# Optimization experiments

Measured on AMD Instinct MI355X. Metric: run time of the kernel, lower is better.

## Reference

```python
import jax, jax.numpy as jnp
import numpy as np
import math

E = 1024   # embed_dim
H = 16     # num_heads
LAT = 1024 # latent_dim
P = LAT // 16  # projectionMatrice output dim (per-head width)
B = 2
S = 2048


def setup_inputs() -> dict:
    key = jax.random.key(0)
    ks = jax.random.split(key, 11)
    sc = 0.02  # small init scale so exp(dot(q_vec, k_vec)) stays finite
    return {
        "x": jax.random.normal(ks[0], (B, S, E), jnp.float32),
        "WQ": jax.random.normal(ks[1], (E, E), jnp.float32) * sc,
        "WK": jax.random.normal(ks[2], (E, E), jnp.float32) * sc,
        "WV": jax.random.normal(ks[3], (E, E), jnp.float32) * sc,
        "result_weight": jax.random.normal(ks[4], (E, E), jnp.float32) * sc,
        "proj_w": jax.random.normal(ks[5], (E, P), jnp.float32) * sc,
        "proj_b": jax.random.normal(ks[6], (P,), jnp.float32) * sc,
        "q1_vector": jax.random.normal(ks[7], (E,), jnp.float32) * sc,
        "k1_vector": jax.random.normal(ks[8], (E,), jnp.float32) * sc,
        "q2_vector": jax.random.normal(ks[9], (E,), jnp.float32) * sc,
        "k2_vector": jax.random.normal(ks[10], (E,), jnp.float32) * sc,
        "lambda_init": jnp.zeros((1,), jnp.float32),
    }


def reference(x, WQ, WK, WV, result_weight, proj_w, proj_b,
              q1_vector, k1_vector, q2_vector, k2_vector, lambda_init):
    head_dim = E // H
    scale = 1.0 / math.sqrt(head_dim)
    # projectionMatrice(x @ W): torch Linear -> x @ proj_w + proj_b with proj_w [E, P]
    q = (x @ WQ) @ proj_w + proj_b   # [B, S, P]
    k = (x @ WK) @ proj_w + proj_b   # [B, S, P]
    v = (x @ WV) @ proj_w + proj_b   # [B, S, P]
    q1, q2 = jnp.split(q, 2, axis=-1)  # [B, S, P/2] each
    k1, k2 = jnp.split(k, 2, axis=-1)
    lam = (jnp.exp(jnp.dot(q1_vector, k1_vector))
           - jnp.exp(jnp.dot(q2_vector, k2_vector)) + lambda_init[0])
    attn1 = jnp.einsum('bsp,btp->bst', q1, k1) * scale  # [B, S, S]
    attn2 = jnp.einsum('bsp,btp->bst', q2, k2) * scale
    base = jnp.einsum('bst,btp->bsp', attn1 - lam * attn2, v)  # [B, S, P]
    # Stateful KV-cache grows by one identical (key, value) copy per head call;
    # head i's tiled-cache output equals (i+1) * base (exact reassociation).
    mult = jnp.arange(1, H + 1, dtype=x.dtype)  # [H]
    heads = (base[:, :, None, :] * mult[None, None, :, None]).reshape(B, S, H * P)  # [B, S, E]
    return heads @ result_weight
```

## Files before the change

kernel.cpp:

```cpp
#include <hip/hip_runtime.h>
#include <hip/hip_bf16.h>


typedef __attribute__((ext_vector_type(8))) short short8;
typedef __attribute__((ext_vector_type(4))) float f32x4;
typedef unsigned short ushort_t;
typedef unsigned int uint_t;

__device__ inline ushort_t f2bf(float v) {
    uint_t u = __float_as_uint(v);
    return (ushort_t)((u + 0x7FFF + ((u >> 16) & 1)) >> 16);
}
__device__ inline float bf2f(ushort_t h) { return __uint_as_float(((uint_t)h) << 16); }
__device__ inline void split2(float v, ushort_t& hi, ushort_t& lo) {
    hi = f2bf(v);
    lo = f2bf(v - bf2f(hi));
}
__device__ inline int swzA(int row, int k) { return (row * 64 + k) ^ ((row & 7) << 3); }

#define WS_PTRS(ws) \
    float* wppartT = (ws); \
    float* qpart   = (ws) + 1572864; \
    float* Mpart   = (ws) + 7864320; \
    float* Weff    = (ws) + 8388608; \
    float* lamp    = (ws) + 8454144; \
    ushort_t* ub   = (ushort_t*)((ws) + 8454160); \
    ushort_t* WpThi = ub; \
    ushort_t* WpTlo = ub + 196608; \
    ushort_t* Qhi   = ub + 393216; \
    ushort_t* Qlo   = ub + 655360; \
    ushort_t* GThi  = ub + 917504; \
    ushort_t* GTlo  = ub + 1048576;

__global__ __launch_bounds__(256) void mla_p1(
    const float* __restrict__ WQ, const float* __restrict__ WK, const float* __restrict__ WV,
    const float* __restrict__ proj_w, const float* __restrict__ RW,
    const float* __restrict__ q1v, const float* __restrict__ k1v,
    const float* __restrict__ q2v, const float* __restrict__ k2v,
    const float* __restrict__ lam0, float* __restrict__ ws)
{
    __shared__ __align__(16) char smem[32768];
    WS_PTRS(ws)
    (void)qpart; (void)Mpart; (void)WpThi; (void)WpTlo; (void)Qhi; (void)Qlo; (void)GThi; (void)GTlo;
    int t = blockIdx.x, tid = threadIdx.x;
    int wave = tid >> 6, lane = tid & 63, rl = lane & 15, kg = lane >> 4;

    if (t < 384) {
        ushort_t* Ah = (ushort_t*)smem;
        ushort_t* Al = (ushort_t*)(smem + 8192);
        ushort_t* Bh = (ushort_t*)(smem + 16384);
        ushort_t* Bl = (ushort_t*)(smem + 24576);
        int slice = t / 48, tt = t % 48, z = tt / 16, rowblk = tt % 16;
        const float* A = ((z == 0) ? WQ : (z == 1) ? WK : WV) + (long long)rowblk * 64 * 1024;
        f32x4 acc[4] = {};
        int k0 = slice * 128;
        for (int ch = 0; ch < 2; ++ch, k0 += 64) {
            #pragma unroll
            for (int i = 0; i < 4; ++i) {
                int pos = tid + 256 * i;
                int r = pos >> 4, k4 = (pos & 15) * 4;
                float4 v = *(const float4*)&A[(long long)r * 1024 + k0 + k4];
                ushort4 h, l;
                split2(v.x, h.x, l.x); split2(v.y, h.y, l.y);
                split2(v.z, h.z, l.z); split2(v.w, h.w, l.w);
                int idx = swzA(r, k4);
                *(ushort4*)&Ah[idx] = h;
                *(ushort4*)&Al[idx] = l;
            }
            #pragma unroll
            for (int i = 0; i < 4; ++i) {
                int pos = tid + 256 * i;
                int kk = pos >> 4, n4 = (pos & 15) * 4;
                float4 v = *(const float4*)&proj_w[(long long)(k0 + kk) * 64 + n4];
                float vv[4] = {v.x, v.y, v.z, v.w};
                #pragma unroll
                for (int j = 0; j < 4; ++j) {
                    ushort_t h, l; split2(vv[j], h, l);
                    int idx = swzA(n4 + j, kk);
                    Bh[idx] = h; Bl[idx] = l;
                }
            }
            __syncthreads();
            int ar = wave * 16 + rl;
            #pragma unroll
            for (int ks = 0; ks < 2; ++ks) {
                int kb = ks * 32 + kg * 8;
                short8 ah = *(const short8*)&Ah[swzA(ar, kb)];
                short8 al = *(const short8*)&Al[swzA(ar, kb)];
                #pragma unroll
                for (int n = 0; n < 4; ++n) {
                    int bi = swzA(n * 16 + rl, kb);
                    short8 bh = *(const short8*)&Bh[bi];
                    short8 bl = *(const short8*)&Bl[bi];
                    acc[n] = __builtin_amdgcn_mfma_f32_16x16x32_bf16(ah, bh, acc[n], 0, 0, 0);
                    acc[n] = __builtin_amdgcn_mfma_f32_16x16x32_bf16(ah, bl, acc[n], 0, 0, 0);
                    acc[n] = __builtin_amdgcn_mfma_f32_16x16x32_bf16(al, bh, acc[n], 0, 0, 0);
                }
            }
            __syncthreads();
        }
        #pragma unroll
        for (int n = 0; n < 4; ++n) {
            int col = n * 16 + rl;
            float4 o = {acc[n][0], acc[n][1], acc[n][2], acc[n][3]};
            long long idx = (long long)slice * 196608 + (long long)(z * 64 + col) * 1024
                          + rowblk * 64 + wave * 16 + kg * 4;
            *(float4*)&wppartT[idx] = o;
        }
    } else if (t < 448) {
        int f4i = (t - 384) * 256 + tid;
        int p = f4i >> 8, e4 = (f4i & 255) * 4;
        float4 s = {0.f, 0.f, 0.f, 0.f};
        #pragma unroll
        for (int h = 0; h < 16; ++h) {
            float4 r = *(const float4*)&RW[(long long)(h * 64 + p) * 1024 + e4];
            float m = (float)(h + 1);
            s.x += m * r.x; s.y += m * r.y; s.z += m * r.z; s.w += m * r.w;
        }
        *(float4*)&Weff[(long long)p * 1024 + e4] = s;
    } else {
        float* red = (float*)smem;
        float d1 = 0.f, d2 = 0.f;
        for (int i = tid; i < 1024; i += 256) {
            d1 += q1v[i] * k1v[i];
            d2 += q2v[i] * k2v[i];
        }
        #pragma unroll
        for (int off = 32; off > 0; off >>= 1) {
            d1 += __shfl_down(d1, off);
            d2 += __shfl_down(d2, off);
        }
        if ((tid & 63) == 0) { red[tid >> 6] = d1; red[4 + (tid >> 6)] = d2; }
        __syncthreads();
        if (tid == 0) {
            float s1 = red[0] + red[1] + red[2] + red[3];
            float s2 = red[4] + red[5] + red[6] + red[7];
            lamp[0] = expf(s1) - expf(s2) + lam0[0];
        }
    }
}

__global__ __launch_bounds__(256) void mla_p2(float* __restrict__ ws)
{
    WS_PTRS(ws)
    (void)qpart; (void)Mpart; (void)Weff; (void)lamp; (void)Qhi; (void)Qlo; (void)GThi; (void)GTlo;
    int idx = blockIdx.x * 256 + threadIdx.x;
    long long off = (long long)idx * 4;
    float4 s = {0.f, 0.f, 0.f, 0.f};
    #pragma unroll
    for (int sl = 0; sl < 8; ++sl) {
        float4 m = *(const float4*)&wppartT[(long long)sl * 196608 + off];
        s.x += m.x; s.y += m.y; s.z += m.z; s.w += m.w;
    }
    ushort4 h, l;
    split2(s.x, h.x, l.x); split2(s.y, h.y, l.y);
    split2(s.z, h.z, l.z); split2(s.w, h.w, l.w);
    *(ushort4*)&WpThi[off] = h;
    *(ushort4*)&WpTlo[off] = l;
}

__global__ __launch_bounds__(256) void mla_p3(const float* __restrict__ x, float* __restrict__ ws)
{
    __shared__ __align__(16) char smem[65536];
    WS_PTRS(ws)
    (void)wppartT; (void)Mpart; (void)Weff; (void)lamp; (void)Qhi; (void)Qlo; (void)GThi; (void)GTlo;
    ushort_t* Ah = (ushort_t*)smem;
    ushort_t* Al = (ushort_t*)(smem + 8192);
    ushort_t (*Bh)[4096] = (ushort_t(*)[4096])(smem + 16384);
    ushort_t (*Bl)[4096] = (ushort_t(*)[4096])(smem + 40960);
    int t = blockIdx.x, tid = threadIdx.x;
    int wave = tid >> 6, lane = tid & 63, rl = lane & 15, kg = lane >> 4;
    int rowblk = t & 63, slice = t >> 6;
    long long row0 = (long long)rowblk * 64;
    f32x4 acc[3][4] = {};
    int k0 = slice * 128;
    for (int ch = 0; ch < 2; ++ch, k0 += 64) {
        #pragma unroll
        for (int i = 0; i < 4; ++i) {
            int pos = tid + 256 * i;
            int r = pos >> 4, k4 = (pos & 15) * 4;
            float4 v = *(const float4*)&x[(row0 + r) * 1024 + k0 + k4];
            ushort4 h, l;
            split2(v.x, h.x, l.x); split2(v.y, h.y, l.y);
            split2(v.z, h.z, l.z); split2(v.w, h.w, l.w);
            int idx = swzA(r, k4);
            *(ushort4*)&Ah[idx] = h;
            *(ushort4*)&Al[idx] = l;
        }
        #pragma unroll
        for (int z = 0; z < 3; ++z) {
            #pragma unroll
            for (int i = 0; i < 2; ++i) {
                int pos = tid + 256 * i;
                int n = pos >> 3, k8 = (pos & 7) * 8;
                int idx = swzA(n, k8);
                long long src = (long long)(z * 64 + n) * 1024 + k0 + k8;
                *(short8*)&Bh[z][idx] = *(const short8*)&WpThi[src];
                *(short8*)&Bl[z][idx] = *(const short8*)&WpTlo[src];
            }
        }
        __syncthreads();
        int ar = wave * 16 + rl;
        #pragma unroll
        for (int ks = 0; ks < 2; ++ks) {
            int kb = ks * 32 + kg * 8;
            short8 ah = *(const short8*)&Ah[swzA(ar, kb)];
            short8 al = *(const short8*)&Al[swzA(ar, kb)];
            #pragma unroll
            for (int z = 0; z < 3; ++z) {
                #pragma unroll
                for (int n = 0; n < 4; ++n) {
                    int bi = swzA(n * 16 + rl, kb);
                    short8 bh = *(const short8*)&Bh[z][bi];
                    short8 bl = *(const short8*)&Bl[z][bi];
                    acc[z][n] = __builtin_amdgcn_mfma_f32_16x16x32_bf16(ah, bh, acc[z][n], 0, 0, 0);
                    acc[z][n] = __builtin_amdgcn_mfma_f32_16x16x32_bf16(ah, bl, acc[z][n], 0, 0, 0);
                    acc[z][n] = __builtin_amdgcn_mfma_f32_16x16x32_bf16(al, bh, acc[z][n], 0, 0, 0);
                }
            }
        }
        __syncthreads();
    }
    #pragma unroll
    for (int z = 0; z < 3; ++z) {
        float* C = qpart + (long long)(slice * 3 + z) * 262144;
        #pragma unroll
        for (int n = 0; n < 4; ++n) {
            int col = n * 16 + rl;
            #pragma unroll
            for (int j = 0; j < 4; ++j) {
                long long row = row0 + wave * 16 + kg * 4 + j;
                C[row * 64 + col] = acc[z][n][j];
            }
        }
    }
}

__global__ __launch_bounds__(256) void mla_p4(const float* __restrict__ proj_b, float* __restrict__ ws)
{
    __shared__ __align__(16) char smem[17408];
    WS_PTRS(ws)
    (void)wppartT; (void)Weff; (void)lamp; (void)WpThi; (void)WpTlo; (void)GThi; (void)GTlo;
    int t = blockIdx.x, tid = threadIdx.x;
    if (t < 128) {
        float (*ksh)[68] = (float(*)[68])smem;
        float (*vsh)[68] = (float(*)[68])(smem + 8704);
        int sc = t & 63, b = t >> 6;
        long long row0 = (long long)b * 2048 + sc * 32;
        #pragma unroll
        for (int i = 0; i < 4; ++i) {
            int pos = tid + 256 * i;
            int arr = pos >> 9, rem = pos & 511;
            int r = rem >> 4, c4 = (rem & 15) * 4;
            float4 s = *(const float4*)&proj_b[c4];
            long long off = (row0 + r) * 64 + c4;
            #pragma unroll
            for (int sl = 0; sl < 8; ++sl) {
                float4 m = *(const float4*)&qpart[(long long)(sl * 3 + 1 + arr) * 262144 + off];
                s.x += m.x; s.y += m.y; s.z += m.z; s.w += m.w;
            }
            if (arr == 0) *(float4*)&ksh[r][c4] = s;
            else          *(float4*)&vsh[r][c4] = s;
        }
        __syncthreads();
        int p = tid & 63, cgi = tid >> 6;
        float macc[16] = {};
        for (int s = 0; s < 32; ++s) {
            float vv = vsh[s][p];
            float4 k0 = *(const float4*)&ksh[s][cgi * 16];
            float4 k1 = *(const float4*)&ksh[s][cgi * 16 + 4];
            float4 k2 = *(const float4*)&ksh[s][cgi * 16 + 8];
            float4 k3 = *(const float4*)&ksh[s][cgi * 16 + 12];
            macc[0] += k0.x * vv;  macc[1] += k0.y * vv;  macc[2] += k0.z * vv;  macc[3] += k0.w * vv;
            macc[4] += k1.x * vv;  macc[5] += k1.y * vv;  macc[6] += k1.z * vv;  macc[7] += k1.w * vv;
            macc[8] += k2.x * vv;  macc[9] += k2.y * vv;  macc[10] += k2.z * vv; macc[11] += k2.w * vv;
            macc[12] += k3.x * vv; macc[13] += k3.y * vv; macc[14] += k3.z * vv; macc[15] += k3.w * vv;
        }
        float* o = Mpart + ((long long)b * 64 + sc) * 4096;
        #pragma unroll
        for (int ci = 0; ci < 16; ++ci)
            o[(cgi * 16 + ci) * 64 + p] = macc[ci];
    } else {
        int qb = t - 128;
        long long row0 = (long long)qb * 128;
        #pragma unroll
        for (int i = 0; i < 8; ++i) {
            int pos = tid + 256 * i;
            int r = pos >> 4, c4 = (pos & 15) * 4;
            float4 s = *(const float4*)&proj_b[c4];
            long long off = (row0 + r) * 64 + c4;
            #pragma unroll
            for (int sl = 0; sl < 8; ++sl) {
                float4 m = *(const float4*)&qpart[(long long)(sl * 3) * 262144 + off];
                s.x += m.x; s.y += m.y; s.z += m.z; s.w += m.w;
            }
            ushort4 h, l;
            split2(s.x, h.x, l.x); split2(s.y, h.y, l.y);
            split2(s.z, h.z, l.z); split2(s.w, h.w, l.w);
            *(ushort4*)&Qhi[off] = h;
            *(ushort4*)&Qlo[off] = l;
        }
    }
}

__global__ __launch_bounds__(256) void mla_p5(float* __restrict__ ws)
{
    __shared__ __align__(16) char smem[34816];
    WS_PTRS(ws)
    (void)wppartT; (void)qpart; (void)WpThi; (void)WpTlo; (void)Qhi; (void)Qlo;
    float (*As)[68] = (float(*)[68])smem;
    float (*Bs)[68] = (float(*)[68])(smem + 17408);
    int t = blockIdx.x, tid = threadIdx.x;
    int colblk = t & 15, b = t >> 4;
    float lam = lamp[0];
    #pragma unroll
    for (int i = 0; i < 4; ++i) {
        int pos = tid + 256 * i;
        int c = pos >> 4, p4 = (pos & 15) * 4;
        float4 s = {0.f, 0.f, 0.f, 0.f};
        #pragma unroll 8
        for (int sc = 0; sc < 64; ++sc) {
            float4 m = *(const float4*)&Mpart[((long long)b * 64 + sc) * 4096 + c * 64 + p4];
            s.x += m.x; s.y += m.y; s.z += m.z; s.w += m.w;
        }
        float coef = 0.125f * (c < 32 ? 1.0f : -lam);
        s.x *= coef; s.y *= coef; s.z *= coef; s.w *= coef;
        *(float4*)&As[c][p4] = s;
    }
    #pragma unroll
    for (int i = 0; i < 4; ++i) {
        int pos = tid + 256 * i;
        int p = pos >> 4, e4 = (pos & 15) * 4;
        *(float4*)&Bs[p][e4] = *(const float4*)&Weff[(long long)p * 1024 + colblk * 64 + e4];
    }
    __syncthreads();
    int tx = tid & 15, ty = tid >> 4;
    float acc[4][4] = {};
    #pragma unroll 4
    for (int kk4 = 0; kk4 < 64; kk4 += 4) {
        float4 a4[4], b4[4];
        #pragma unroll
        for (int i = 0; i < 4; ++i) a4[i] = *(const float4*)&As[ty * 4 + i][kk4];
        #pragma unroll
        for (int r = 0; r < 4; ++r) b4[r] = *(const float4*)&Bs[kk4 + r][tx * 4];
        #pragma unroll
        for (int i = 0; i < 4; ++i) {
            acc[i][0] += a4[i].x * b4[0].x + a4[i].y * b4[1].x + a4[i].z * b4[2].x + a4[i].w * b4[3].x;
            acc[i][1] += a4[i].x * b4[0].y + a4[i].y * b4[1].y + a4[i].z * b4[2].y + a4[i].w * b4[3].y;
            acc[i][2] += a4[i].x * b4[0].z + a4[i].y * b4[1].z + a4[i].z * b4[2].z + a4[i].w * b4[3].z;
            acc[i][3] += a4[i].x * b4[0].w + a4[i].y * b4[1].w + a4[i].z * b4[2].w + a4[i].w * b4[3].w;
        }
    }
    #pragma unroll
    for (int i = 0; i < 4; ++i)
        #pragma unroll
        for (int j = 0; j < 4; ++j) {
            ushort_t h, l; split2(acc[i][j], h, l);
            long long idx = (long long)b * 65536 + (long long)(colblk * 64 + tx * 4 + j) * 64 + ty * 4 + i;
            GThi[idx] = h; GTlo[idx] = l;
        }
}

__global__ __launch_bounds__(256) void mla_p6(float* __restrict__ ws, float* __restrict__ out)
{
    __shared__ __align__(16) char smem[32768];
    WS_PTRS(ws)
    (void)wppartT; (void)qpart; (void)Mpart; (void)Weff; (void)lamp; (void)WpThi; (void)WpTlo;
    ushort_t* Ah = (ushort_t*)smem;
    ushort_t* Al = (ushort_t*)(smem + 8192);
    ushort_t* Bh = (ushort_t*)(smem + 16384);
    ushort_t* Bl = (ushort_t*)(smem + 24576);
    int t = blockIdx.x, tid = threadIdx.x;
    int wave = tid >> 6, lane = tid & 63, rl = lane & 15, kg = lane >> 4;
    int rowblk = t & 31, colblk = (t >> 5) & 15, b = t >> 9;
    long long row0 = (long long)b * 2048 + rowblk * 64;
    #pragma unroll
    for (int i = 0; i < 2; ++i) {
        int pos = tid + 256 * i;
        int n = pos >> 3, k8 = (pos & 7) * 8;
        int idx = swzA(n, k8);
        long long qsrc = (row0 + n) * 64 + k8;
        long long gsrc = (long long)b * 65536 + (long long)(colblk * 64 + n) * 64 + k8;
        *(short8*)&Ah[idx] = *(const short8*)&Qhi[qsrc];
        *(short8*)&Al[idx] = *(const short8*)&Qlo[qsrc];
        *(short8*)&Bh[idx] = *(const short8*)&GThi[gsrc];
        *(short8*)&Bl[idx] = *(const short8*)&GTlo[gsrc];
    }
    __syncthreads();
    f32x4 acc[4] = {};
    int ar = wave * 16 + rl;
    #pragma unroll
    for (int ks = 0; ks < 2; ++ks) {
        int kb = ks * 32 + kg * 8;
        short8 ah = *(const short8*)&Ah[swzA(ar, kb)];
        short8 al = *(const short8*)&Al[swzA(ar, kb)];
        #pragma unroll
        for (int n = 0; n < 4; ++n) {
            int bi = swzA(n * 16 + rl, kb);
            short8 bh = *(const short8*)&Bh[bi];
            short8 bl = *(const short8*)&Bl[bi];
            acc[n] = __builtin_amdgcn_mfma_f32_16x16x32_bf16(ah, bh, acc[n], 0, 0, 0);
            acc[n] = __builtin_amdgcn_mfma_f32_16x16x32_bf16(ah, bl, acc[n], 0, 0, 0);
            acc[n] = __builtin_amdgcn_mfma_f32_16x16x32_bf16(al, bh, acc[n], 0, 0, 0);
        }
    }
    #pragma unroll
    for (int n = 0; n < 4; ++n) {
        int col = colblk * 64 + n * 16 + rl;
        #pragma unroll
        for (int j = 0; j < 4; ++j) {
            int row = rowblk * 64 + wave * 16 + kg * 4 + j;
            out[(long long)b * 2097152 + (long long)row * 1024 + col] = acc[n][j];
        }
    }
}

extern "C" void kernel_launch(void* const* d_in, const int* in_sizes, int n_in,
                              void* d_out, int out_size, void* d_ws, size_t ws_size,
                              hipStream_t stream)
{
    const float* x      = (const float*)d_in[0];
    const float* WQ     = (const float*)d_in[1];
    const float* WK     = (const float*)d_in[2];
    const float* WV     = (const float*)d_in[3];
    const float* RW     = (const float*)d_in[4];
    const float* proj_w = (const float*)d_in[5];
    const float* proj_b = (const float*)d_in[6];
    const float* q1v    = (const float*)d_in[7];
    const float* k1v    = (const float*)d_in[8];
    const float* q2v    = (const float*)d_in[9];
    const float* k2v    = (const float*)d_in[10];
    const float* lam0   = (const float*)d_in[11];
    float* ws  = (float*)d_ws;
    float* out = (float*)d_out;

    dim3 blk(256);
    mla_p1<<<dim3(449), blk, 0, stream>>>(WQ, WK, WV, proj_w, RW,
                                          q1v, k1v, q2v, k2v, lam0, ws);
    mla_p2<<<dim3(192), blk, 0, stream>>>(ws);
    mla_p3<<<dim3(512), blk, 0, stream>>>(x, ws);
    mla_p4<<<dim3(160), blk, 0, stream>>>(proj_b, ws);
    mla_p5<<<dim3(32), blk, 0, stream>>>(ws);
    mla_p6<<<dim3(1024), blk, 0, stream>>>(ws, out);
}
```

Before: 67.62 us.

## Rebalance kernel split, prefetch QKV projection tiles into registers, halve split-K slices

The Wp^T reduction moves into the same launch as the Weff and lambda work, and the first kernel keeps only the WQ/WK/WV×proj_w split-K GEMM. The x·Wp GEMM now uses 4 K-slices of 256 instead of 8 of 128, and it prefetches the next x and Wp tiles into registers while MFMAs run on the current tile. The M-partial kernel now covers 64 rows per block, which halves the number of partials that the G kernel reduces. Fewer, larger blocks cut partial-sum traffic and expose load latency less often, but they reduce parallelism across CUs and add register pressure.

```diff
diff --git a/kernel.cpp b/kernel.cpp
--- a/kernel.cpp
+++ b/kernel.cpp
@@ -21,10 +21,10 @@
 #define WS_PTRS(ws) \
     float* wppartT = (ws); \
     float* qpart   = (ws) + 1572864; \
-    float* Mpart   = (ws) + 7864320; \
-    float* Weff    = (ws) + 8388608; \
-    float* lamp    = (ws) + 8454144; \
-    ushort_t* ub   = (ushort_t*)((ws) + 8454160); \
+    float* Mpart   = (ws) + 4718592; \
+    float* Weff    = (ws) + 4980736; \
+    float* lamp    = (ws) + 5046272; \
+    ushort_t* ub   = (ushort_t*)((ws) + 5046288); \
     ushort_t* WpThi = ub; \
     ushort_t* WpTlo = ub + 196608; \
     ushort_t* Qhi   = ub + 393216; \
@@ -32,154 +32,30 @@
     ushort_t* GThi  = ub + 917504; \
     ushort_t* GTlo  = ub + 1048576;
 
-__global__ __launch_bounds__(256) void mla_p1(
+__global__ __launch_bounds__(256) void prep_sk(
     const float* __restrict__ WQ, const float* __restrict__ WK, const float* __restrict__ WV,
-    const float* __restrict__ proj_w, const float* __restrict__ RW,
-    const float* __restrict__ q1v, const float* __restrict__ k1v,
-    const float* __restrict__ q2v, const float* __restrict__ k2v,
-    const float* __restrict__ lam0, float* __restrict__ ws)
-{
-    __shared__ __align__(16) char smem[32768];
-    WS_PTRS(ws)
-    (void)qpart; (void)Mpart; (void)WpThi; (void)WpTlo; (void)Qhi; (void)Qlo; (void)GThi; (void)GTlo;
-    int t = blockIdx.x, tid = threadIdx.x;
-    int wave = tid >> 6, lane = tid & 63, rl = lane & 15, kg = lane >> 4;
-
-    if (t < 384) {
-        ushort_t* Ah = (ushort_t*)smem;
-        ushort_t* Al = (ushort_t*)(smem + 8192);
-        ushort_t* Bh = (ushort_t*)(smem + 16384);
-        ushort_t* Bl = (ushort_t*)(smem + 24576);
-        int slice = t / 48, tt = t % 48, z = tt / 16, rowblk = tt % 16;
-        const float* A = ((z == 0) ? WQ : (z == 1) ? WK : WV) + (long long)rowblk * 64 * 1024;
-        f32x4 acc[4] = {};
-        int k0 = slice * 128;
-        for (int ch = 0; ch < 2; ++ch, k0 += 64) {
-            #pragma unroll
-            for (int i = 0; i < 4; ++i) {
-                int pos = tid + 256 * i;
-                int r = pos >> 4, k4 = (pos & 15) * 4;
-                float4 v = *(const float4*)&A[(long long)r * 1024 + k0 + k4];
-                ushort4 h, l;
-                split2(v.x, h.x, l.x); split2(v.y, h.y, l.y);
-                split2(v.z, h.z, l.z); split2(v.w, h.w, l.w);
-                int idx = swzA(r, k4);
-                *(ushort4*)&Ah[idx] = h;
-                *(ushort4*)&Al[idx] = l;
-            }
-            #pragma unroll
-            for (int i = 0; i < 4; ++i) {
-                int pos = tid + 256 * i;
-                int kk = pos >> 4, n4 = (pos & 15) * 4;
-                float4 v = *(const float4*)&proj_w[(long long)(k0 + kk) * 64 + n4];
-                float vv[4] = {v.x, v.y, v.z, v.w};
-                #pragma unroll
-                for (int j = 0; j < 4; ++j) {
-                    ushort_t h, l; split2(vv[j], h, l);
-                    int idx = swzA(n4 + j, kk);
-                    Bh[idx] = h; Bl[idx] = l;
-                }
-            }
-            __syncthreads();
-            int ar = wave * 16 + rl;
-            #pragma unroll
-            for (int ks = 0; ks < 2; ++ks) {
-                int kb = ks * 32 + kg * 8;
-                short8 ah = *(const short8*)&Ah[swzA(ar, kb)];
-                short8 al = *(const short8*)&Al[swzA(ar, kb)];
-                #pragma unroll
-                for (int n = 0; n < 4; ++n) {
-                    int bi = swzA(n * 16 + rl, kb);
-                    short8 bh = *(const short8*)&Bh[bi];
-                    short8 bl = *(const short8*)&Bl[bi];
-                    acc[n] = __builtin_amdgcn_mfma_f32_16x16x32_bf16(ah, bh, acc[n], 0, 0, 0);
-                    acc[n] = __builtin_amdgcn_mfma_f32_16x16x32_bf16(ah, bl, acc[n], 0, 0, 0);
-                    acc[n] = __builtin_amdgcn_mfma_f32_16x16x32_bf16(al, bh, acc[n], 0, 0, 0);
-                }
-            }
-            __syncthreads();
-        }
-        #pragma unroll
-        for (int n = 0; n < 4; ++n) {
-            int col = n * 16 + rl;
-            float4 o = {acc[n][0], acc[n][1], acc[n][2], acc[n][3]};
-            long long idx = (long long)slice * 196608 + (long long)(z * 64 + col) * 1024
-                          + rowblk * 64 + wave * 16 + kg * 4;
-            *(float4*)&wppartT[idx] = o;
-        }
-    } else if (t < 448) {
-        int f4i = (t - 384) * 256 + tid;
-        int p = f4i >> 8, e4 = (f4i & 255) * 4;
-        float4 s = {0.f, 0.f, 0.f, 0.f};
-        #pragma unroll
-        for (int h = 0; h < 16; ++h) {
-            float4 r = *(const float4*)&RW[(long long)(h * 64 + p) * 1024 + e4];
-            float m = (float)(h + 1);
-            s.x += m * r.x; s.y += m * r.y; s.z += m * r.z; s.w += m * r.w;
-        }
-        *(float4*)&Weff[(long long)p * 1024 + e4] = s;
-    } else {
-        float* red = (float*)smem;
-        float d1 = 0.f, d2 = 0.f;
-        for (int i = tid; i < 1024; i += 256) {
-            d1 += q1v[i] * k1v[i];
-            d2 += q2v[i] * k2v[i];
-        }
-        #pragma unroll
-        for (int off = 32; off > 0; off >>= 1) {
-            d1 += __shfl_down(d1, off);
-            d2 += __shfl_down(d2, off);
-        }
-        if ((tid & 63) == 0) { red[tid >> 6] = d1; red[4 + (tid >> 6)] = d2; }
-        __syncthreads();
-        if (tid == 0) {
-            float s1 = red[0] + red[1] + red[2] + red[3];
-            float s2 = red[4] + red[5] + red[6] + red[7];
-            lamp[0] = expf(s1) - expf(s2) + lam0[0];
-        }
-    }
-}
-
-__global__ __launch_bounds__(256) void mla_p2(float* __restrict__ ws)
-{
-    WS_PTRS(ws)
-    (void)qpart; (void)Mpart; (void)Weff; (void)lamp; (void)Qhi; (void)Qlo; (void)GThi; (void)GTlo;
-    int idx = blockIdx.x * 256 + threadIdx.x;
-    long long off = (long long)idx * 4;
-    float4 s = {0.f, 0.f, 0.f, 0.f};
-    #pragma unroll
-    for (int sl = 0; sl < 8; ++sl) {
-        float4 m = *(const float4*)&wppartT[(long long)sl * 196608 + off];
-        s.x += m.x; s.y += m.y; s.z += m.z; s.w += m.w;
-    }
-    ushort4 h, l;
-    split2(s.x, h.x, l.x); split2(s.y, h.y, l.y);
-    split2(s.z, h.z, l.z); split2(s.w, h.w, l.w);
-    *(ushort4*)&WpThi[off] = h;
-    *(ushort4*)&WpTlo[off] = l;
-}
-
-__global__ __launch_bounds__(256) void mla_p3(const float* __restrict__ x, float* __restrict__ ws)
-{
-    __shared__ __align__(16) char smem[65536];
-    WS_PTRS(ws)
-    (void)wppartT; (void)Mpart; (void)Weff; (void)lamp; (void)Qhi; (void)Qlo; (void)GThi; (void)GTlo;
-    ushort_t* Ah = (ushort_t*)smem;
-    ushort_t* Al = (ushort_t*)(smem + 8192);
-    ushort_t (*Bh)[4096] = (ushort_t(*)[4096])(smem + 16384);
-    ushort_t (*Bl)[4096] = (ushort_t(*)[4096])(smem + 40960);
-    int t = blockIdx.x, tid = threadIdx.x;
-    int wave = tid >> 6, lane = tid & 63, rl = lane & 15, kg = lane >> 4;
-    int rowblk = t & 63, slice = t >> 6;
-    long long row0 = (long long)rowblk * 64;
-    f32x4 acc[3][4] = {};
+    const float* __restrict__ proj_w, float* __restrict__ ws)
+{
+    __shared__ __align__(16) ushort_t Ah[4096], Al[4096], Bh[4096], Bl[4096];
+    WS_PTRS(ws)
+    (void)qpart; (void)Mpart; (void)Weff; (void)lamp;
+    (void)WpThi; (void)WpTlo; (void)Qhi; (void)Qlo; (void)GThi; (void)GTlo;
+    int bid = blockIdx.x;
+    int slice = bid / 48, t = bid % 48, z = t / 16, rowblk = t % 16;
+    const float* A = ((z == 0) ? WQ : (z == 1) ? WK : WV) + (long long)rowblk * 64 * 1024;
+
+    int tid = threadIdx.x;
+    int wave = tid >> 6, lane = tid & 63;
+    int rl = lane & 15, kg = lane >> 4;
+    f32x4 acc[4] = {};
+
     int k0 = slice * 128;
     for (int ch = 0; ch < 2; ++ch, k0 += 64) {
         #pragma unroll
         for (int i = 0; i < 4; ++i) {
             int pos = tid + 256 * i;
             int r = pos >> 4, k4 = (pos & 15) * 4;
-            float4 v = *(const float4*)&x[(row0 + r) * 1024 + k0 + k4];
+            float4 v = *(const float4*)&A[(long long)r * 1024 + k0 + k4];
             ushort4 h, l;
             split2(v.x, h.x, l.x); split2(v.y, h.y, l.y);
             split2(v.z, h.z, l.z); split2(v.w, h.w, l.w);
@@ -188,18 +64,181 @@
             *(ushort4*)&Al[idx] = l;
         }
         #pragma unroll
-        for (int z = 0; z < 3; ++z) {
+        for (int i = 0; i < 4; ++i) {
+            int pos = tid + 256 * i;
+            int kk = pos >> 4, n4 = (pos & 15) * 4;
+            float4 v = *(const float4*)&proj_w[(long long)(k0 + kk) * 64 + n4];
+            float vv[4] = {v.x, v.y, v.z, v.w};
+            #pragma unroll
+            for (int j = 0; j < 4; ++j) {
+                ushort_t h, l; split2(vv[j], h, l);
+                int idx = swzA(n4 + j, kk);
+                Bh[idx] = h; Bl[idx] = l;
+            }
+        }
+        __syncthreads();
+        int ar = wave * 16 + rl;
+        #pragma unroll
+        for (int ks = 0; ks < 2; ++ks) {
+            int kb = ks * 32 + kg * 8;
+            short8 ah = *(const short8*)&Ah[swzA(ar, kb)];
+            short8 al = *(const short8*)&Al[swzA(ar, kb)];
+            #pragma unroll
+            for (int n = 0; n < 4; ++n) {
+                int bi = swzA(n * 16 + rl, kb);
+                short8 bh = *(const short8*)&Bh[bi];
+                short8 bl = *(const short8*)&Bl[bi];
+                acc[n] = __builtin_amdgcn_mfma_f32_16x16x32_bf16(ah, bh, acc[n], 0, 0, 0);
+                acc[n] = __builtin_amdgcn_mfma_f32_16x16x32_bf16(ah, bl, acc[n], 0, 0, 0);
+                acc[n] = __builtin_amdgcn_mfma_f32_16x16x32_bf16(al, bh, acc[n], 0, 0, 0);
+            }
+        }
+        __syncthreads();
+    }
+    #pragma unroll
+    for (int n = 0; n < 4; ++n) {
+        int col = n * 16 + rl;
+        float4 o = {acc[n][0], acc[n][1], acc[n][2], acc[n][3]};
+        long long idx = (long long)slice * 196608 + (long long)(z * 64 + col) * 1024
+                      + rowblk * 64 + wave * 16 + kg * 4;
+        *(float4*)&wppartT[idx] = o;
+    }
+}
+
+__global__ __launch_bounds__(256) void wpfix2x(
+    const float* __restrict__ RW,
+    const float* __restrict__ q1v, const float* __restrict__ k1v,
+    const float* __restrict__ q2v, const float* __restrict__ k2v,
+    const float* __restrict__ lam0, float* __restrict__ ws)
+{
+    __shared__ float red[2][4];
+    WS_PTRS(ws)
+    (void)qpart; (void)Mpart; (void)Qhi; (void)Qlo; (void)GThi; (void)GTlo;
+    int t = blockIdx.x, tid = threadIdx.x;
+    if (t < 192) {
+        int idx = t * 256 + tid;
+        long long off = (long long)idx * 4;
+        float4 s = {0.f, 0.f, 0.f, 0.f};
+        #pragma unroll
+        for (int sl = 0; sl < 8; ++sl) {
+            float4 m = *(const float4*)&wppartT[(long long)sl * 196608 + off];
+            s.x += m.x; s.y += m.y; s.z += m.z; s.w += m.w;
+        }
+        ushort4 h, l;
+        split2(s.x, h.x, l.x); split2(s.y, h.y, l.y);
+        split2(s.z, h.z, l.z); split2(s.w, h.w, l.w);
+        *(ushort4*)&WpThi[off] = h;
+        *(ushort4*)&WpTlo[off] = l;
+    } else if (t < 256) {
+        int f4i = (t - 192) * 256 + tid;
+        int p = f4i >> 8, e4 = (f4i & 255) * 4;
+        float4 s = {0.f, 0.f, 0.f, 0.f};
+        #pragma unroll
+        for (int h = 0; h < 16; ++h) {
+            float4 r = *(const float4*)&RW[(long long)(h * 64 + p) * 1024 + e4];
+            float m = (float)(h + 1);
+            s.x += m * r.x; s.y += m * r.y; s.z += m * r.z; s.w += m * r.w;
+        }
+        *(float4*)&Weff[(long long)p * 1024 + e4] = s;
+    } else {
+        float d1 = 0.f, d2 = 0.f;
+        for (int i = tid; i < 1024; i += 256) {
+            d1 += q1v[i] * k1v[i];
+            d2 += q2v[i] * k2v[i];
+        }
+        #pragma unroll
+        for (int off = 32; off > 0; off >>= 1) {
+            d1 += __shfl_down(d1, off);
+            d2 += __shfl_down(d2, off);
+        }
+        if ((tid & 63) == 0) { red[0][tid >> 6] = d1; red[1][tid >> 6] = d2; }
+        __syncthreads();
+        if (tid == 0) {
+            float s1 = red[0][0] + red[0][1] + red[0][2] + red[0][3];
+            float s2 = red[1][0] + red[1][1] + red[1][2] + red[1][3];
+            lamp[0] = expf(s1) - expf(s2) + lam0[0];
+        }
+    }
+}
+
+__global__ __launch_bounds__(256) void qkv_f(
+    const float* __restrict__ x, float* __restrict__ ws)
+{
+    __shared__ __align__(16) char smem[65536];
+    WS_PTRS(ws)
+    (void)wppartT; (void)Mpart; (void)Weff; (void)lamp; (void)Qhi; (void)Qlo; (void)GThi; (void)GTlo;
+    ushort_t* Ah = (ushort_t*)smem;
+    ushort_t* Al = (ushort_t*)(smem + 8192);
+    ushort_t (*Bh)[4096] = (ushort_t(*)[4096])(smem + 16384);
+    ushort_t (*Bl)[4096] = (ushort_t(*)[4096])(smem + 40960);
+    int bid = blockIdx.x, tid = threadIdx.x;
+    int wave = tid >> 6, lane = tid & 63, rl = lane & 15, kg = lane >> 4;
+    int rowblk = bid & 63, slice = bid >> 6;
+    long long row0 = (long long)rowblk * 64;
+    f32x4 acc[3][4] = {};
+
+    float4 av[4];
+    short8 pbh[3][2], pbl[3][2];
+    int k0 = slice * 256;
+    #pragma unroll
+    for (int i = 0; i < 4; ++i) {
+        int pos = tid + 256 * i;
+        int r = pos >> 4, k4 = (pos & 15) * 4;
+        av[i] = *(const float4*)&x[(row0 + r) * 1024 + k0 + k4];
+    }
+    #pragma unroll
+    for (int z = 0; z < 3; ++z)
+        #pragma unroll
+        for (int i = 0; i < 2; ++i) {
+            int pos = tid + 256 * i;
+            int n = pos >> 3, k8 = (pos & 7) * 8;
+            long long src = (long long)(z * 64 + n) * 1024 + k0 + k8;
+            pbh[z][i] = *(const short8*)&WpThi[src];
+            pbl[z][i] = *(const short8*)&WpTlo[src];
+        }
+
+    for (int ch = 0; ch < 4; ++ch) {
+        #pragma unroll
+        for (int i = 0; i < 4; ++i) {
+            int pos = tid + 256 * i;
+            int r = pos >> 4, k4 = (pos & 15) * 4;
+            ushort4 h, l;
+            split2(av[i].x, h.x, l.x); split2(av[i].y, h.y, l.y);
+            split2(av[i].z, h.z, l.z); split2(av[i].w, h.w, l.w);
+            int idx = swzA(r, k4);
+            *(ushort4*)&Ah[idx] = h;
+            *(ushort4*)&Al[idx] = l;
+        }
+        #pragma unroll
+        for (int z = 0; z < 3; ++z)
             #pragma unroll
             for (int i = 0; i < 2; ++i) {
                 int pos = tid + 256 * i;
                 int n = pos >> 3, k8 = (pos & 7) * 8;
                 int idx = swzA(n, k8);
-                long long src = (long long)(z * 64 + n) * 1024 + k0 + k8;
-                *(short8*)&Bh[z][idx] = *(const short8*)&WpThi[src];
-                *(short8*)&Bl[z][idx] = *(const short8*)&WpTlo[src];
-            }
-        }
+                *(short8*)&Bh[z][idx] = pbh[z][i];
+                *(short8*)&Bl[z][idx] = pbl[z][i];
+            }
         __syncthreads();
+        if (ch < 3) {
+            int kn = k0 + (ch + 1) * 64;
+            #pragma unroll
+            for (int i = 0; i < 4; ++i) {
+                int pos = tid + 256 * i;
+                int r = pos >> 4, k4 = (pos & 15) * 4;
+                av[i] = *(const float4*)&x[(row0 + r) * 1024 + kn + k4];
+            }
+            #pragma unroll
+            for (int z = 0; z < 3; ++z)
+                #pragma unroll
+                for (int i = 0; i < 2; ++i) {
+                    int pos = tid + 256 * i;
+                    int n = pos >> 3, k8 = (pos & 7) * 8;
+                    long long src = (long long)(z * 64 + n) * 1024 + kn + k8;
+                    pbh[z][i] = *(const short8*)&WpThi[src];
+                    pbl[z][i] = *(const short8*)&WpTlo[src];
+                }
+        }
         int ar = wave * 16 + rl;
         #pragma unroll
         for (int ks = 0; ks < 2; ++ks) {
@@ -219,7 +258,7 @@
                 }
             }
         }
-        __syncthreads();
+        __builtin_amdgcn_s_barrier();
     }
     #pragma unroll
     for (int z = 0; z < 3; ++z) {
@@ -236,26 +275,27 @@
     }
 }
 
-__global__ __launch_bounds__(256) void mla_p4(const float* __restrict__ proj_b, float* __restrict__ ws)
-{
-    __shared__ __align__(16) char smem[17408];
+__global__ __launch_bounds__(256) void mpartq(
+    const float* __restrict__ proj_b, float* __restrict__ ws)
+{
+    __shared__ __align__(16) char smem[34816];
     WS_PTRS(ws)
     (void)wppartT; (void)Weff; (void)lamp; (void)WpThi; (void)WpTlo; (void)GThi; (void)GTlo;
     int t = blockIdx.x, tid = threadIdx.x;
-    if (t < 128) {
+    if (t < 64) {
         float (*ksh)[68] = (float(*)[68])smem;
-        float (*vsh)[68] = (float(*)[68])(smem + 8704);
-        int sc = t & 63, b = t >> 6;
-        long long row0 = (long long)b * 2048 + sc * 32;
-        #pragma unroll
-        for (int i = 0; i < 4; ++i) {
-            int pos = tid + 256 * i;
-            int arr = pos >> 9, rem = pos & 511;
+        float (*vsh)[68] = (float(*)[68])(smem + 17408);
+        int ks = t & 31, b = t >> 5;
+        long long row0 = (long long)b * 2048 + ks * 64;
+        #pragma unroll
+        for (int i = 0; i < 8; ++i) {
+            int pos = tid + 256 * i;
+            int arr = pos >> 10, rem = pos & 1023;
             int r = rem >> 4, c4 = (rem & 15) * 4;
             float4 s = *(const float4*)&proj_b[c4];
             long long off = (row0 + r) * 64 + c4;
             #pragma unroll
-            for (int sl = 0; sl < 8; ++sl) {
+            for (int sl = 0; sl < 4; ++sl) {
                 float4 m = *(const float4*)&qpart[(long long)(sl * 3 + 1 + arr) * 262144 + off];
                 s.x += m.x; s.y += m.y; s.z += m.z; s.w += m.w;
             }
@@ -265,7 +305,7 @@
         __syncthreads();
         int p = tid & 63, cgi = tid >> 6;
         float macc[16] = {};
-        for (int s = 0; s < 32; ++s) {
+        for (int s = 0; s < 64; ++s) {
             float vv = vsh[s][p];
             float4 k0 = *(const float4*)&ksh[s][cgi * 16];
             float4 k1 = *(const float4*)&ksh[s][cgi * 16 + 4];
@@ -276,12 +316,12 @@
             macc[8] += k2.x * vv;  macc[9] += k2.y * vv;  macc[10] += k2.z * vv; macc[11] += k2.w * vv;
             macc[12] += k3.x * vv; macc[13] += k3.y * vv; macc[14] += k3.z * vv; macc[15] += k3.w * vv;
         }
-        float* o = Mpart + ((long long)b * 64 + sc) * 4096;
+        float* o = Mpart + (long long)b * 131072 + (long long)ks * 4096;
         #pragma unroll
         for (int ci = 0; ci < 16; ++ci)
             o[(cgi * 16 + ci) * 64 + p] = macc[ci];
     } else {
-        int qb = t - 128;
+        int qb = t - 64;
         long long row0 = (long long)qb * 128;
         #pragma unroll
         for (int i = 0; i < 8; ++i) {
@@ -290,7 +330,7 @@
             float4 s = *(const float4*)&proj_b[c4];
             long long off = (row0 + r) * 64 + c4;
             #pragma unroll
-            for (int sl = 0; sl < 8; ++sl) {
+            for (int sl = 0; sl < 4; ++sl) {
                 float4 m = *(const float4*)&qpart[(long long)(sl * 3) * 262144 + off];
                 s.x += m.x; s.y += m.y; s.z += m.z; s.w += m.w;
             }
@@ -303,13 +343,11 @@
     }
 }
 
-__global__ __launch_bounds__(256) void mla_p5(float* __restrict__ ws)
-{
-    __shared__ __align__(16) char smem[34816];
+__global__ __launch_bounds__(256) void gkern(float* __restrict__ ws)
+{
+    __shared__ float As[64][68], Bs[64][68];
     WS_PTRS(ws)
     (void)wppartT; (void)qpart; (void)WpThi; (void)WpTlo; (void)Qhi; (void)Qlo;
-    float (*As)[68] = (float(*)[68])smem;
-    float (*Bs)[68] = (float(*)[68])(smem + 17408);
     int t = blockIdx.x, tid = threadIdx.x;
     int colblk = t & 15, b = t >> 4;
     float lam = lamp[0];
@@ -319,8 +357,8 @@
         int c = pos >> 4, p4 = (pos & 15) * 4;
         float4 s = {0.f, 0.f, 0.f, 0.f};
         #pragma unroll 8
-        for (int sc = 0; sc < 64; ++sc) {
-            float4 m = *(const float4*)&Mpart[((long long)b * 64 + sc) * 4096 + c * 64 + p4];
+        for (int sc = 0; sc < 32; ++sc) {
+            float4 m = *(const float4*)&Mpart[(long long)b * 131072 + (long long)sc * 4096 + c * 64 + p4];
             s.x += m.x; s.y += m.y; s.z += m.z; s.w += m.w;
         }
         float coef = 0.125f * (c < 32 ? 1.0f : -lam);
@@ -361,19 +399,17 @@
         }
 }
 
-__global__ __launch_bounds__(256) void mla_p6(float* __restrict__ ws, float* __restrict__ out)
-{
-    __shared__ __align__(16) char smem[32768];
-    WS_PTRS(ws)
-    (void)wppartT; (void)qpart; (void)Mpart; (void)Weff; (void)lamp; (void)WpThi; (void)WpTlo;
-    ushort_t* Ah = (ushort_t*)smem;
-    ushort_t* Al = (ushort_t*)(smem + 8192);
-    ushort_t* Bh = (ushort_t*)(smem + 16384);
-    ushort_t* Bl = (ushort_t*)(smem + 24576);
-    int t = blockIdx.x, tid = threadIdx.x;
-    int wave = tid >> 6, lane = tid & 63, rl = lane & 15, kg = lane >> 4;
-    int rowblk = t & 31, colblk = (t >> 5) & 15, b = t >> 9;
+__global__ __launch_bounds__(256) void outk(float* __restrict__ ws, float* __restrict__ out)
+{
+    __shared__ __align__(16) ushort_t Ah[4096], Al[4096], Bh[4096], Bl[4096];
+    WS_PTRS(ws)
+    (void)wppartT; (void)qpart; (void)Mpart; (void)Weff; (void)lamp;
+    (void)WpThi; (void)WpTlo;
+    int bid = blockIdx.x;
+    int rowblk = bid & 31, colblk = (bid >> 5) & 15, b = bid >> 9;
+    int tid = threadIdx.x;
     long long row0 = (long long)b * 2048 + rowblk * 64;
+
     #pragma unroll
     for (int i = 0; i < 2; ++i) {
         int pos = tid + 256 * i;
@@ -387,6 +423,9 @@
         *(short8*)&Bl[idx] = *(const short8*)&GTlo[gsrc];
     }
     __syncthreads();
+
+    int wave = tid >> 6, lane = tid & 63;
+    int rl = lane & 15, kg = lane >> 4;
     f32x4 acc[4] = {};
     int ar = wave * 16 + rl;
     #pragma unroll
@@ -435,11 +474,10 @@
     float* out = (float*)d_out;
 
     dim3 blk(256);
-    mla_p1<<<dim3(449), blk, 0, stream>>>(WQ, WK, WV, proj_w, RW,
-                                          q1v, k1v, q2v, k2v, lam0, ws);
-    mla_p2<<<dim3(192), blk, 0, stream>>>(ws);
-    mla_p3<<<dim3(512), blk, 0, stream>>>(x, ws);
-    mla_p4<<<dim3(160), blk, 0, stream>>>(proj_b, ws);
-    mla_p5<<<dim3(32), blk, 0, stream>>>(ws);
-    mla_p6<<<dim3(1024), blk, 0, stream>>>(ws, out);
-}
+    prep_sk<<<dim3(384), blk, 0, stream>>>(WQ, WK, WV, proj_w, ws);
+    wpfix2x<<<dim3(257), blk, 0, stream>>>(RW, q1v, k1v, q2v, k2v, lam0, ws);
+    qkv_f<<<dim3(256), blk, 0, stream>>>(x, ws);
+    mpartq<<<dim3(96), blk, 0, stream>>>(proj_b, ws);
+    gkern<<<dim3(32), blk, 0, stream>>>(ws);
+    outk<<<dim3(1024), blk, 0, stream>>>(ws, out);
+}
```

Measured after the change: 61.28 us. 1.1x faster.
